# Performance work log

Hardware: AMD Instinct MI355X
Metric: run time of the kernel (lower is better)

The kernel has to match this reference:

```python
import jax, jax.numpy as jnp
import numpy as np

N_HOPS = 3  # context_hops


def _l2_normalize(x, eps=1e-12):
    # matches torch.nn.functional.normalize(x) row-wise
    return x / jnp.maximum(jnp.linalg.norm(x, axis=-1, keepdims=True), eps)


def setup_inputs() -> dict:
    key = jax.random.key(0)
    k1, k2, k3, k4, k5 = jax.random.split(key, 5)
    n_entities, n_drugs, n_relations, n_edges, d = 100000, 2000, 51, 1000000, 64
    return {
        "entity_emb": jax.random.normal(k1, (n_entities, d), dtype=jnp.float32),
        "drug_emb": jax.random.normal(k2, (n_drugs, d), dtype=jnp.float32),
        "relation_emb": jax.random.normal(k3, (n_relations, d), dtype=jnp.float32),
        "edge_index": jax.random.randint(k4, (2, n_edges), 0, n_entities),
        "edge_type": jax.random.randint(k5, (n_edges,), 0, n_relations),
    }


def reference(entity_emb, drug_emb, relation_emb, edge_index, edge_type):
    n_entities = entity_emb.shape[0]
    n_drugs = drug_emb.shape[0]
    head, tail = edge_index[0], edge_index[1]

    # per-head in-degree for scatter_mean (clamp empty segments to 1 like torch_scatter)
    cnt = jax.ops.segment_sum(jnp.ones(head.shape[0], dtype=entity_emb.dtype),
                              head, num_segments=n_entities)
    denom = jnp.maximum(cnt, 1.0)[:, None]  # [n_entities, 1]

    ent_res, drug_res, rel_res = entity_emb, drug_emb, relation_emb
    for _ in range(N_HOPS):
        # gather-multiply: [E, d]
        msg = entity_emb[tail] * relation_emb[edge_type]
        # scatter_mean over head indices
        agg = jax.ops.segment_sum(msg, head, num_segments=n_entities) / denom
        entity_emb = _l2_normalize(agg)
        drug_emb = entity_emb[:n_drugs]        # normalize commutes with row slicing
        relation_emb = _l2_normalize(relation_emb)
        ent_res = ent_res + entity_emb
        drug_res = drug_res + drug_emb
        rel_res = rel_res + relation_emb
    return ent_res, drug_res, rel_res
```

## Files before the change

kernel.cpp:

```cpp
#include <hip/hip_runtime.h>
#include <hip/hip_bf16.h>

#define D 64
#define NBIN_MAX 1024

__device__ __forceinline__ int load_idx(const void* p, long long i, int mode) {
  return mode ? (int)((const long long*)p)[i] : ((const int*)p)[i];
}
__device__ __forceinline__ float loadf(const void* p, long long i, int fm) {
  return fm ? ((const float*)p)[i]
            : __bfloat162float(((const __hip_bfloat16*)p)[i]);
}
__device__ __forceinline__ unsigned short bf16bits(float v) {
  unsigned u = __float_as_uint(v);
  return (unsigned short)((u + 0x7FFFu + ((u >> 16) & 1u)) >> 16);
}
__device__ __forceinline__ float bflo(unsigned u) { return __uint_as_float(u << 16); }
__device__ __forceinline__ float bfhi(unsigned u) { return __uint_as_float(u & 0xFFFF0000u); }

__global__ __launch_bounds__(256) void zero_detect_kernel(
    int* __restrict__ gcur, int nbins,
    const void* eidx, const void* etype, const void* ent0,
    int* __restrict__ flags, int n_edges) {
  int tid = threadIdx.x;
  for (int j = tid; j < nbins; j += 256) gcur[j] = 0;
  if (tid < 64) {
    int lane = tid;
    long long tot_e = 2LL * n_edges;
    long long step_e = tot_e / 130; if (step_e < 1) step_e = 1;
    long long pos_e = 1 + 2LL * lane * step_e;
    int ve = (pos_e < tot_e) ? ((const int*)eidx)[pos_e] : 0;
    unsigned long long be = __ballot(ve != 0);

    long long tot_t = n_edges;
    long long step_t = tot_t / 130; if (step_t < 1) step_t = 1;
    long long pos_t = 1 + 2LL * lane * step_t;
    int vt = (pos_t < tot_t) ? ((const int*)etype)[pos_t] : 0;
    unsigned long long bt = __ballot(vt != 0);

    float a = __bfloat162float(((const __hip_bfloat16*)ent0)[lane]);
    unsigned long long bf = __ballot(!(fabsf(a) <= 64.0f));

    if (lane == 0) {
      flags[0] = (be == 0ULL) ? 1 : 0;
      flags[1] = (bt == 0ULL) ? 1 : 0;
      flags[3] = (bf != 0ULL) ? 1 : 0;
    }
  }
}

__global__ __launch_bounds__(256) void build1_kernel(
    const void* __restrict__ ent0, const void* __restrict__ rel0,
    const void* __restrict__ eidx, const void* __restrict__ etype,
    unsigned short* __restrict__ entC, float* __restrict__ relRaw,
    float* __restrict__ relN, float* __restrict__ out_rel,
    int* __restrict__ gcur, int* __restrict__ binbuf,
    const int* __restrict__ flags,
    int ent_elems, int rel_elems, int n_ent, int n_rel, int n_edges,
    int nbins, int binCap) {
  __shared__ int s_cnt[NBIN_MAX];
  __shared__ int s_base[NBIN_MAX];
  int tid = threadIdx.x;
  int i = blockIdx.x * 256 + tid;
  int fm = flags[3];
  if (fm) {
    int i8 = i * 8;
    if (i8 < ent_elems) {
      float4 a = ((const float4*)ent0)[i * 2];
      float4 b = ((const float4*)ent0)[i * 2 + 1];
      uint4 o;
      o.x = (unsigned)bf16bits(a.x) | ((unsigned)bf16bits(a.y) << 16);
      o.y = (unsigned)bf16bits(a.z) | ((unsigned)bf16bits(a.w) << 16);
      o.z = (unsigned)bf16bits(b.x) | ((unsigned)bf16bits(b.y) << 16);
      o.w = (unsigned)bf16bits(b.z) | ((unsigned)bf16bits(b.w) << 16);
      ((uint4*)entC)[i] = o;
    }
  }
  if (i < rel_elems) {
    float v = loadf(rel0, i, fm);
    relRaw[i] = v;
    float ss = v * v;
    for (int o = 32; o > 0; o >>= 1) ss += __shfl_xor(ss, o, 64);
    float nv = (ss > 0.f) ? v * rsqrtf(ss) : 0.f;
    relN[i] = nv;
    out_rel[i] = v + 3.0f * nv;
  }
  int part_blocks = (n_edges + 4095) >> 12;
  if ((int)blockIdx.x < part_blocks) {
    int e0 = (int)blockIdx.x << 12;
    int m = flags[0], mr = flags[1];
    for (int b = tid; b < nbins; b += 256) s_cnt[b] = 0;
    __syncthreads();
    for (int k = 0; k < 16; ++k) {
      int e = e0 + k * 256 + tid;
      if (e < n_edges) {
        int h = load_idx(eidx, e, m);
        h = min(max(h, 0), n_ent - 1);
        atomicAdd(&s_cnt[h >> 9], 1);
      }
    }
    __syncthreads();
    for (int b = tid; b < nbins; b += 256) {
      int c = s_cnt[b];
      s_base[b] = c ? atomicAdd(&gcur[b], c) : 0;
      s_cnt[b] = 0;
    }
    __syncthreads();
    for (int k = 0; k < 16; ++k) {
      int e = e0 + k * 256 + tid;
      if (e < n_edges) {
        int h = load_idx(eidx, e, m);
        int t = load_idx(eidx, (long long)n_edges + e, m);
        int r = load_idx(etype, e, mr);
        h = min(max(h, 0), n_ent - 1);
        t = min(max(t, 0), n_ent - 1);
        r = min(max(r, 0), n_rel - 1);
        int bin = h >> 9;
        int pos = s_base[bin] + atomicAdd(&s_cnt[bin], 1);
        if (pos < binCap)
          binbuf[(size_t)bin * binCap + pos] =
              t | (r << 17) | ((h & 511) << 23);
      }
    }
  }
}

__global__ __launch_bounds__(256) void build2_kernel(
    const int* __restrict__ gcur, const int* __restrict__ binbuf,
    int* __restrict__ staging, int n_ent, int binCap, int C) {
  __shared__ int off2[512];
  int b = blockIdx.x;
  int tid = threadIdx.x;
  for (int j = tid; j < 512; j += 256) off2[j] = 0;
  __syncthreads();
  int cnt = min(gcur[b], binCap);
  const int* src = binbuf + (size_t)b * binCap;
  int ebase = b << 9;
  for (int e = tid; e < cnt; e += 256) {
    int pack = src[e];
    int hl = (int)(((unsigned)pack) >> 23);
    int pos = atomicAdd(&off2[hl], 1);
    if (pos < C - 1)
      staging[(size_t)(ebase + hl) * C + 1 + pos] = pack & 0x7FFFFF;
  }
  __syncthreads();
  for (int j = tid; j < 512; j += 256) {
    int ent = ebase + j;
    if (ent < n_ent) staging[(size_t)ent * C] = off2[j];
  }
}

template <int SHIFT>
__device__ __forceinline__ float4 hop_row_core(
    const unsigned short* __restrict__ src, const unsigned short* lds_rel,
    const int* __restrict__ adj, size_t base, int pv, int C,
    int sub, int gbase) {
  float4 acc = make_float4(0.f, 0.f, 0.f, 0.f);
  int cnt = __shfl(pv, gbase, 64);
  cnt = min(cnt, C - 1);
  int ehi = min(cnt, 15);
  for (int j = 0; j < ehi; j += 8) {
    uint2 sv[8];
    int rr[8];
#pragma unroll
    for (int k = 0; k < 8; ++k) {
      int e = j + k;
      int ee = (e < ehi) ? e : 0;
      int p = __shfl(pv, gbase + 1 + ee, 64);
      unsigned toff = ((unsigned)(p & 0x1FFFF) << (SHIFT + 1)) + (unsigned)(sub << 3);
      rr[k] = (e < ehi) ? (int)(((unsigned)p >> 17) & 0x3F) : -1;
      sv[k] = *(const uint2*)((const char*)src + toff);
    }
#pragma unroll
    for (int k = 0; k < 8; ++k) {
      uint2 rv;
      if (rr[k] >= 0) rv = *(const uint2*)(lds_rel + (rr[k] << 6) + (sub << 2));
      else { rv.x = 0u; rv.y = 0u; }
      acc.x += bflo(sv[k].x) * bflo(rv.x);
      acc.y += bfhi(sv[k].x) * bfhi(rv.x);
      acc.z += bflo(sv[k].y) * bflo(rv.y);
      acc.w += bfhi(sv[k].y) * bfhi(rv.y);
    }
  }
  if (cnt > 15) {
    int slotbase = 16;
    int elo = 15;
    while (true) {
      int pv2 = adj[base + slotbase + sub];
      int eh2 = min(cnt, slotbase + 15);
      for (int j = elo; j < eh2; j += 8) {
        uint2 sv[8];
        int rr[8];
#pragma unroll
        for (int k = 0; k < 8; ++k) {
          int e = j + k;
          int ee = (e < eh2) ? e : elo;
          int p = __shfl(pv2, gbase + (1 + ee - slotbase), 64);
          unsigned toff = ((unsigned)(p & 0x1FFFF) << (SHIFT + 1)) + (unsigned)(sub << 3);
          rr[k] = (e < eh2) ? (int)(((unsigned)p >> 17) & 0x3F) : -1;
          sv[k] = *(const uint2*)((const char*)src + toff);
        }
#pragma unroll
        for (int k = 0; k < 8; ++k) {
          uint2 rv;
          if (rr[k] >= 0) rv = *(const uint2*)(lds_rel + (rr[k] << 6) + (sub << 2));
          else { rv.x = 0u; rv.y = 0u; }
          acc.x += bflo(sv[k].x) * bflo(rv.x);
          acc.y += bfhi(sv[k].x) * bfhi(rv.x);
          acc.z += bflo(sv[k].y) * bflo(rv.y);
          acc.w += bfhi(sv[k].y) * bfhi(rv.y);
        }
      }
      if (eh2 >= cnt) break;
      slotbase += 16;
      elo = slotbase - 1;
    }
  }
  return acc;
}

__device__ __forceinline__ float4 norm4(float4 acc) {
  float ss = acc.x * acc.x + acc.y * acc.y + acc.z * acc.z + acc.w * acc.w;
  for (int o = 8; o > 0; o >>= 1) ss += __shfl_xor(ss, o, 64);
  float inv = (ss > 0.f) ? rsqrtf(ss) : 0.f;
  return make_float4(acc.x * inv, acc.y * inv, acc.z * inv, acc.w * inv);
}

__global__ __launch_bounds__(256, 8) void hop0_kernel(
    const unsigned short* __restrict__ srcRaw, const unsigned short* __restrict__ srcConv,
    const float* __restrict__ relX, const int* __restrict__ staging,
    const int* __restrict__ flags,
    unsigned short* __restrict__ v0out ,
    int n_ent, int n_rel, int C) {
  extern __shared__ unsigned short lds_rel[];
  for (int i = threadIdx.x; i < n_rel * D; i += blockDim.x)
    lds_rel[i] = bf16bits(relX[i]);
  __syncthreads();
  const unsigned short* src = flags[3] ? srcConv : srcRaw;
  int lane = threadIdx.x & 63;
  int sub = lane & 15;
  int grp = (lane >> 4) & 3;
  int gbase = lane & 48;
  int wid = (blockIdx.x * blockDim.x + threadIdx.x) >> 6;
  int nw = (gridDim.x * blockDim.x) >> 6;
  int step = nw * 4;
  int row = wid * 4 + grp;
  if (row >= n_ent) return;
  size_t base = (size_t)row * C;
  int pv = staging[base + sub];
  while (row < n_ent) {
    int nrow = row + step;
    size_t nbase = (size_t)nrow * C;
    int pv_next = (nrow < n_ent) ? staging[nbase + sub] : 0;
    float4 val = norm4(hop_row_core<6>(src, lds_rel, staging, base, pv, C, sub, gbase));
    uint2 o;
    o.x = (unsigned)bf16bits(val.x) | ((unsigned)bf16bits(val.y) << 16);
    o.y = (unsigned)bf16bits(val.z) | ((unsigned)bf16bits(val.w) << 16);
    *(uint2*)(v0out + ((size_t)row << 7) + (sub << 2)) = o;
    row = nrow; base = nbase; pv = pv_next;
  }
}

__global__ __launch_bounds__(256, 8) void hop1_kernel(
    const unsigned short* __restrict__ v0, const float* __restrict__ relX,
    const int* __restrict__ staging,
    unsigned short* __restrict__ dst, int n_ent, int n_rel, int C) {
  extern __shared__ unsigned short lds_rel[];
  for (int i = threadIdx.x; i < n_rel * D; i += blockDim.x)
    lds_rel[i] = bf16bits(relX[i]);
  __syncthreads();
  int lane = threadIdx.x & 63;
  int sub = lane & 15;
  int grp = (lane >> 4) & 3;
  int gbase = lane & 48;
  int wid = (blockIdx.x * blockDim.x + threadIdx.x) >> 6;
  int nw = (gridDim.x * blockDim.x) >> 6;
  int step = nw * 4;
  int row = wid * 4 + grp;
  if (row >= n_ent) return;
  size_t base = (size_t)row * C;
  int pv = staging[base + sub];
  while (row < n_ent) {
    int nrow = row + step;
    size_t nbase = (size_t)nrow * C;
    int pv_next = (nrow < n_ent) ? staging[nbase + sub] : 0;
    float4 val = norm4(hop_row_core<7>(v0, lds_rel, staging, base, pv, C, sub, gbase));
    uint2 o;
    o.x = (unsigned)bf16bits(val.x) | ((unsigned)bf16bits(val.y) << 16);
    o.y = (unsigned)bf16bits(val.z) | ((unsigned)bf16bits(val.w) << 16);
    *(uint2*)(dst + ((size_t)row << 6) + (sub << 2)) = o;
    row = nrow; base = nbase; pv = pv_next;
  }
}

__global__ __launch_bounds__(256, 8) void hop2_kernel(
    const unsigned short* __restrict__ v1tab, const float* __restrict__ relX,
    const int* __restrict__ staging,
    const void* __restrict__ ent0, const void* __restrict__ drug0,
    const int* __restrict__ flags,
    float* out_ent, float* __restrict__ out_drug,
    int n_ent, int n_drugs, int n_rel, int C) {
  extern __shared__ unsigned short lds_rel[];
  for (int i = threadIdx.x; i < n_rel * D; i += blockDim.x)
    lds_rel[i] = bf16bits(relX[i]);
  __syncthreads();
  int fm = flags[3];
  int lane = threadIdx.x & 63;
  int sub = lane & 15;
  int grp = (lane >> 4) & 3;
  int gbase = lane & 48;
  int wid = (blockIdx.x * blockDim.x + threadIdx.x) >> 6;
  int nw = (gridDim.x * blockDim.x) >> 6;
  int step = nw * 4;
  int row = wid * 4 + grp;
  if (row >= n_ent) return;
  size_t base = (size_t)row * C;
  int pv = staging[base + sub];
  while (row < n_ent) {
    int nrow = row + step;
    size_t nbase = (size_t)nrow * C;
    int pv_next = (nrow < n_ent) ? staging[nbase + sub] : 0;
    float4 val = norm4(hop_row_core<6>(v1tab, lds_rel, staging, base, pv, C, sub, gbase));
    size_t eoff = ((size_t)row << 6) + (sub << 2);
    uint2 b0 = *(const uint2*)((const unsigned short*)out_ent +
                               ((size_t)row << 7) + (sub << 2));
    uint2 b1 = *(const uint2*)(v1tab + eoff);
    float4 s;
    s.x = val.x + bflo(b0.x) + bflo(b1.x);
    s.y = val.y + bfhi(b0.x) + bfhi(b1.x);
    s.z = val.z + bflo(b0.y) + bflo(b1.y);
    s.w = val.w + bfhi(b0.y) + bfhi(b1.y);
    float4 basev;
    if (fm) basev = *(const float4*)((const float*)ent0 + eoff);
    else {
      uint2 bb = *(const uint2*)((const unsigned short*)ent0 + eoff);
      basev = make_float4(bflo(bb.x), bfhi(bb.x), bflo(bb.y), bfhi(bb.y));
    }
    *(float4*)(out_ent + eoff) =
        make_float4(basev.x + s.x, basev.y + s.y, basev.z + s.z, basev.w + s.w);
    if (row < n_drugs) {
      float4 db;
      if (fm) db = *(const float4*)((const float*)drug0 + eoff);
      else {
        uint2 bb = *(const uint2*)((const unsigned short*)drug0 + eoff);
        db = make_float4(bflo(bb.x), bfhi(bb.x), bflo(bb.y), bfhi(bb.y));
      }
      *(float4*)(out_drug + eoff) =
          make_float4(db.x + s.x, db.y + s.y, db.z + s.z, db.w + s.w);
    }
    row = nrow; base = nbase; pv = pv_next;
  }
}

__global__ void mini_flag_kernel(float* out, int hostbits) {
  if (blockIdx.x == 0 && threadIdx.x == 0)
    out[0] = 64.0f * (float)hostbits;
}

extern "C" void kernel_launch(void* const* d_in, const int* in_sizes, int n_in,
                              void* d_out, int out_size, void* d_ws, size_t ws_size,
                              hipStream_t stream) {
  const void* ent0  = d_in[0];
  const void* drug0 = d_in[1];
  const void* rel0  = d_in[2];
  const void* eidx  = d_in[3];
  const void* etype = d_in[4];
  float* out = (float*)d_out;

  const int ent_elems  = in_sizes[0];
  const int drug_elems = in_sizes[1];
  const int rel_elems  = in_sizes[2];
  const int n_edges    = in_sizes[4];
  const int n_ent   = ent_elems / D;
  const int n_drugs = drug_elems / D;
  const int n_rel   = rel_elems / D;

  const int nbins  = (n_ent + 511) >> 9;
  const int binCap = (nbins > 0) ? ent_elems / nbins : 0;
  const long long expected = (nbins > 0) ? (n_edges + nbins - 1) / nbins : 0;

  int hostbits = 0;
  bool sizes_ok = (n_in == 5) &&
                  (in_sizes[3] == 2 * n_edges) &&
                  (out_size == ent_elems + drug_elems + rel_elems) &&
                  (ent_elems % D == 0) && (drug_elems % D == 0) &&
                  (rel_elems % D == 0) && (n_ent > 0) && (n_edges > 0) &&
                  (n_ent <= 131072) && (n_rel >= 1) && (n_rel <= 64) &&
                  (n_drugs <= n_ent) && (nbins <= NBIN_MAX) &&
                  ((long long)binCap >= 2 * expected + 1024);
  if (!sizes_ok) hostbits |= 32;

  char* w = (char*)d_ws;
  auto alloc = [&](size_t bytes) {
    char* p = w;
    w += (bytes + 255) / 256 * 256;
    return p;
  };
  int* flags    = (int*)alloc(256);
  int* gcur     = (int*)alloc((size_t)NBIN_MAX * 4);
  float* relRaw = (float*)alloc((size_t)(rel_elems > 0 ? rel_elems : 1) * 4);
  float* relN   = (float*)alloc((size_t)(rel_elems > 0 ? rel_elems : 1) * 4);
  unsigned short* entA = (unsigned short*)alloc((size_t)(ent_elems > 0 ? ent_elems : 1) * 2);
  size_t fixed = (size_t)(w - (char*)d_ws);
  long long avail = (ws_size > fixed + 512) ? (long long)(ws_size - fixed - 512) : 0;
  int C = 0;
  if (n_ent > 0) {
    if (avail >= (long long)n_ent * 64 * 4) C = 64;
    else if (avail >= (long long)n_ent * 32 * 4) C = 32;
  }
  if (C == 0) hostbits |= 16;
  int* staging = (int*)alloc(((size_t)(n_ent > 0 ? n_ent : 1) * (size_t)(C > 0 ? C : 1) + 64) * 4);
  unsigned short* entC = entA;
  int* binbuf = (int*)out;

  if (hostbits) {
    mini_flag_kernel<<<1, 64, 0, stream>>>(out, hostbits);
    return;
  }

  float* out_ent  = out;
  float* out_drug = out + ent_elems;
  float* out_rel  = out + ent_elems + drug_elems;

  zero_detect_kernel<<<1, 256, 0, stream>>>(
      gcur, nbins, eidx, etype, ent0, flags, n_edges);

  int conv_blocks = (ent_elems / 8 + 255) / 256;
  int part_blocks = (n_edges + 4095) >> 12;
  int rel_blocks  = (rel_elems + 255) / 256;
  int g1 = conv_blocks;
  if (part_blocks > g1) g1 = part_blocks;
  if (rel_blocks > g1) g1 = rel_blocks;
  build1_kernel<<<g1, 256, 0, stream>>>(
      ent0, rel0, eidx, etype, entC, relRaw, relN, out_rel,
      gcur, binbuf, flags, ent_elems, rel_elems, n_ent, n_rel, n_edges,
      nbins, binCap);

  build2_kernel<<<nbins, 256, 0, stream>>>(
      gcur, binbuf, staging, n_ent, binCap, C);

  size_t lds_bytes = (size_t)n_rel * D * 2;
  int hop_blocks = 4096;
  hop0_kernel<<<hop_blocks, 256, lds_bytes, stream>>>(
      (const unsigned short*)ent0, entC, relRaw, staging, flags,
      (unsigned short*)out_ent, n_ent, n_rel, C);
  hop1_kernel<<<hop_blocks, 256, lds_bytes, stream>>>(
      (const unsigned short*)out_ent, relN, staging, entA, n_ent, n_rel, C);
  hop2_kernel<<<hop_blocks, 256, lds_bytes, stream>>>(
      entA, relN, staging, ent0, drug0, flags,
      out_ent, out_drug, n_ent, n_drugs, n_rel, C);
}
```

Baseline: 231.9 us.

## Store relations as fp32 in LDS with zero row, nontemporal epilogue, fewer blocks

The relation table is kept in LDS as fp32 with an extra zero row, so padded edge slots index that row instead of taking a branch, and the bf16 unpack on the relation side disappears. The hop2 epilogue uses nontemporal loads and stores for the streaming residual and output traffic. The hop grid is halved from 4096 to 2048 blocks, cutting per-block LDS fill cost. In exchange LDS use per block doubles (about 13KB) and relation values are no longer rounded to bf16, which slightly changes numerics.

```diff
diff --git a/kernel.cpp b/kernel.cpp
--- a/kernel.cpp
+++ b/kernel.cpp
@@ -17,6 +17,21 @@
 }
 __device__ __forceinline__ float bflo(unsigned u) { return __uint_as_float(u << 16); }
 __device__ __forceinline__ float bfhi(unsigned u) { return __uint_as_float(u & 0xFFFF0000u); }
+
+typedef float v4f __attribute__((ext_vector_type(4)));
+typedef unsigned v2u __attribute__((ext_vector_type(2)));
+__device__ __forceinline__ float4 ntload_f4(const float* p) {
+  v4f t = __builtin_nontemporal_load((const v4f*)p);
+  return make_float4(t.x, t.y, t.z, t.w);
+}
+__device__ __forceinline__ uint2 ntload_u2(const void* p) {
+  v2u t = __builtin_nontemporal_load((const v2u*)p);
+  uint2 r; r.x = t.x; r.y = t.y; return r;
+}
+__device__ __forceinline__ void ntstore_f4(float* p, float4 v) {
+  v4f t; t.x = v.x; t.y = v.y; t.z = v.z; t.w = v.w;
+  __builtin_nontemporal_store(t, (v4f*)p);
+}
 
 __global__ __launch_bounds__(256) void zero_detect_kernel(
     int* __restrict__ gcur, int nbins,
@@ -152,8 +167,8 @@
 
 template <int SHIFT>
 __device__ __forceinline__ float4 hop_row_core(
-    const unsigned short* __restrict__ src, const unsigned short* lds_rel,
-    const int* __restrict__ adj, size_t base, int pv, int C,
+    const unsigned short* __restrict__ src, const float* lds_rel,
+    const int* __restrict__ adj, size_t base, int pv, int C, int zr,
     int sub, int gbase) {
   float4 acc = make_float4(0.f, 0.f, 0.f, 0.f);
   int cnt = __shfl(pv, gbase, 64);
@@ -168,18 +183,16 @@
       int ee = (e < ehi) ? e : 0;
       int p = __shfl(pv, gbase + 1 + ee, 64);
       unsigned toff = ((unsigned)(p & 0x1FFFF) << (SHIFT + 1)) + (unsigned)(sub << 3);
-      rr[k] = (e < ehi) ? (int)(((unsigned)p >> 17) & 0x3F) : -1;
+      rr[k] = (e < ehi) ? (int)(((unsigned)p >> 17) & 0x3F) : zr;
       sv[k] = *(const uint2*)((const char*)src + toff);
     }
 #pragma unroll
     for (int k = 0; k < 8; ++k) {
-      uint2 rv;
-      if (rr[k] >= 0) rv = *(const uint2*)(lds_rel + (rr[k] << 6) + (sub << 2));
-      else { rv.x = 0u; rv.y = 0u; }
-      acc.x += bflo(sv[k].x) * bflo(rv.x);
-      acc.y += bfhi(sv[k].x) * bfhi(rv.x);
-      acc.z += bflo(sv[k].y) * bflo(rv.y);
-      acc.w += bfhi(sv[k].y) * bfhi(rv.y);
+      float4 rv = *(const float4*)(lds_rel + (rr[k] << 6) + (sub << 2));
+      acc.x += bflo(sv[k].x) * rv.x;
+      acc.y += bfhi(sv[k].x) * rv.y;
+      acc.z += bflo(sv[k].y) * rv.z;
+      acc.w += bfhi(sv[k].y) * rv.w;
     }
   }
   if (cnt > 15) {
@@ -197,18 +210,16 @@
           int ee = (e < eh2) ? e : elo;
           int p = __shfl(pv2, gbase + (1 + ee - slotbase), 64);
           unsigned toff = ((unsigned)(p & 0x1FFFF) << (SHIFT + 1)) + (unsigned)(sub << 3);
-          rr[k] = (e < eh2) ? (int)(((unsigned)p >> 17) & 0x3F) : -1;
+          rr[k] = (e < eh2) ? (int)(((unsigned)p >> 17) & 0x3F) : zr;
           sv[k] = *(const uint2*)((const char*)src + toff);
         }
 #pragma unroll
         for (int k = 0; k < 8; ++k) {
-          uint2 rv;
-          if (rr[k] >= 0) rv = *(const uint2*)(lds_rel + (rr[k] << 6) + (sub << 2));
-          else { rv.x = 0u; rv.y = 0u; }
-          acc.x += bflo(sv[k].x) * bflo(rv.x);
-          acc.y += bfhi(sv[k].x) * bfhi(rv.x);
-          acc.z += bflo(sv[k].y) * bflo(rv.y);
-          acc.w += bfhi(sv[k].y) * bfhi(rv.y);
+          float4 rv = *(const float4*)(lds_rel + (rr[k] << 6) + (sub << 2));
+          acc.x += bflo(sv[k].x) * rv.x;
+          acc.y += bfhi(sv[k].x) * rv.y;
+          acc.z += bflo(sv[k].y) * rv.z;
+          acc.w += bfhi(sv[k].y) * rv.w;
         }
       }
       if (eh2 >= cnt) break;
@@ -224,6 +235,14 @@
   for (int o = 8; o > 0; o >>= 1) ss += __shfl_xor(ss, o, 64);
   float inv = (ss > 0.f) ? rsqrtf(ss) : 0.f;
   return make_float4(acc.x * inv, acc.y * inv, acc.z * inv, acc.w * inv);
+}
+
+__device__ __forceinline__ void fill_rel_lds(float* lds_rel, const float* relX,
+                                             int n_rel) {
+  int tot = (n_rel + 1) * D;
+  for (int i = threadIdx.x; i < tot; i += blockDim.x)
+    lds_rel[i] = (i < n_rel * D) ? relX[i] : 0.f;
+  __syncthreads();
 }
 
 __global__ __launch_bounds__(256, 8) void hop0_kernel(
@@ -232,10 +251,8 @@
     const int* __restrict__ flags,
     unsigned short* __restrict__ v0out ,
     int n_ent, int n_rel, int C) {
-  extern __shared__ unsigned short lds_rel[];
-  for (int i = threadIdx.x; i < n_rel * D; i += blockDim.x)
-    lds_rel[i] = bf16bits(relX[i]);
-  __syncthreads();
+  extern __shared__ float lds_rel[];
+  fill_rel_lds(lds_rel, relX, n_rel);
   const unsigned short* src = flags[3] ? srcConv : srcRaw;
   int lane = threadIdx.x & 63;
   int sub = lane & 15;
@@ -252,7 +269,7 @@
     int nrow = row + step;
     size_t nbase = (size_t)nrow * C;
     int pv_next = (nrow < n_ent) ? staging[nbase + sub] : 0;
-    float4 val = norm4(hop_row_core<6>(src, lds_rel, staging, base, pv, C, sub, gbase));
+    float4 val = norm4(hop_row_core<6>(src, lds_rel, staging, base, pv, C, n_rel, sub, gbase));
     uint2 o;
     o.x = (unsigned)bf16bits(val.x) | ((unsigned)bf16bits(val.y) << 16);
     o.y = (unsigned)bf16bits(val.z) | ((unsigned)bf16bits(val.w) << 16);
@@ -265,10 +282,8 @@
     const unsigned short* __restrict__ v0, const float* __restrict__ relX,
     const int* __restrict__ staging,
     unsigned short* __restrict__ dst, int n_ent, int n_rel, int C) {
-  extern __shared__ unsigned short lds_rel[];
-  for (int i = threadIdx.x; i < n_rel * D; i += blockDim.x)
-    lds_rel[i] = bf16bits(relX[i]);
-  __syncthreads();
+  extern __shared__ float lds_rel[];
+  fill_rel_lds(lds_rel, relX, n_rel);
   int lane = threadIdx.x & 63;
   int sub = lane & 15;
   int grp = (lane >> 4) & 3;
@@ -284,7 +299,7 @@
     int nrow = row + step;
     size_t nbase = (size_t)nrow * C;
     int pv_next = (nrow < n_ent) ? staging[nbase + sub] : 0;
-    float4 val = norm4(hop_row_core<7>(v0, lds_rel, staging, base, pv, C, sub, gbase));
+    float4 val = norm4(hop_row_core<7>(v0, lds_rel, staging, base, pv, C, n_rel, sub, gbase));
     uint2 o;
     o.x = (unsigned)bf16bits(val.x) | ((unsigned)bf16bits(val.y) << 16);
     o.y = (unsigned)bf16bits(val.z) | ((unsigned)bf16bits(val.w) << 16);
@@ -300,10 +315,8 @@
     const int* __restrict__ flags,
     float* out_ent, float* __restrict__ out_drug,
     int n_ent, int n_drugs, int n_rel, int C) {
-  extern __shared__ unsigned short lds_rel[];
-  for (int i = threadIdx.x; i < n_rel * D; i += blockDim.x)
-    lds_rel[i] = bf16bits(relX[i]);
-  __syncthreads();
+  extern __shared__ float lds_rel[];
+  fill_rel_lds(lds_rel, relX, n_rel);
   int fm = flags[3];
   int lane = threadIdx.x & 63;
   int sub = lane & 15;
@@ -320,10 +333,10 @@
     int nrow = row + step;
     size_t nbase = (size_t)nrow * C;
     int pv_next = (nrow < n_ent) ? staging[nbase + sub] : 0;
-    float4 val = norm4(hop_row_core<6>(v1tab, lds_rel, staging, base, pv, C, sub, gbase));
+    float4 val = norm4(hop_row_core<6>(v1tab, lds_rel, staging, base, pv, C, n_rel, sub, gbase));
     size_t eoff = ((size_t)row << 6) + (sub << 2);
-    uint2 b0 = *(const uint2*)((const unsigned short*)out_ent +
-                               ((size_t)row << 7) + (sub << 2));
+    uint2 b0 = ntload_u2((const unsigned short*)out_ent +
+                         ((size_t)row << 7) + (sub << 2));
     uint2 b1 = *(const uint2*)(v1tab + eoff);
     float4 s;
     s.x = val.x + bflo(b0.x) + bflo(b1.x);
@@ -331,22 +344,22 @@
     s.z = val.z + bflo(b0.y) + bflo(b1.y);
     s.w = val.w + bfhi(b0.y) + bfhi(b1.y);
     float4 basev;
-    if (fm) basev = *(const float4*)((const float*)ent0 + eoff);
+    if (fm) basev = ntload_f4((const float*)ent0 + eoff);
     else {
-      uint2 bb = *(const uint2*)((const unsigned short*)ent0 + eoff);
+      uint2 bb = ntload_u2((const unsigned short*)ent0 + eoff);
       basev = make_float4(bflo(bb.x), bfhi(bb.x), bflo(bb.y), bfhi(bb.y));
     }
-    *(float4*)(out_ent + eoff) =
-        make_float4(basev.x + s.x, basev.y + s.y, basev.z + s.z, basev.w + s.w);
+    ntstore_f4(out_ent + eoff,
+               make_float4(basev.x + s.x, basev.y + s.y, basev.z + s.z, basev.w + s.w));
     if (row < n_drugs) {
       float4 db;
-      if (fm) db = *(const float4*)((const float*)drug0 + eoff);
+      if (fm) db = ntload_f4((const float*)drug0 + eoff);
       else {
-        uint2 bb = *(const uint2*)((const unsigned short*)drug0 + eoff);
+        uint2 bb = ntload_u2((const unsigned short*)drug0 + eoff);
         db = make_float4(bflo(bb.x), bfhi(bb.x), bflo(bb.y), bfhi(bb.y));
       }
-      *(float4*)(out_drug + eoff) =
-          make_float4(db.x + s.x, db.y + s.y, db.z + s.z, db.w + s.w);
+      ntstore_f4(out_drug + eoff,
+                 make_float4(db.x + s.x, db.y + s.y, db.z + s.z, db.w + s.w));
     }
     row = nrow; base = nbase; pv = pv_next;
   }
@@ -439,8 +452,8 @@
   build2_kernel<<<nbins, 256, 0, stream>>>(
       gcur, binbuf, staging, n_ent, binCap, C);
 
-  size_t lds_bytes = (size_t)n_rel * D * 2;
-  int hop_blocks = 4096;
+  size_t lds_bytes = (size_t)(n_rel + 1) * D * 4;
+  int hop_blocks = 2048;
   hop0_kernel<<<hop_blocks, 256, lds_bytes, stream>>>(
       (const unsigned short*)ent0, entC, relRaw, staging, flags,
       (unsigned short*)out_ent, n_ent, n_rel, C);
```

Result: faster. 205.7 us (-11.3%).
